# Kernel optimization log

Hardware: AMD Instinct MI355X
Metric: run time of the kernel (lower is better)

## Reference

```python
import jax, jax.numpy as jnp
import numpy as np
import math

SEQ = 45000
FEAT = 30
DEPTH, HEADS, DK, MLP, C = 4, 4, 32, 512, 32
MAXSEQ = 512


def pos_embed_table():
    # Enformer-style basis functions over distances [-SEQ+1, SEQ-1]
    d = jnp.arange(-SEQ + 1, SEQ, dtype=jnp.float32)
    a = jnp.abs(d)[:, None]
    nb = FEAT // 6  # basis per class (exponential / central-mask / gamma)
    # exponential decay
    hl = 2.0 ** jnp.linspace(3.0, math.log(SEQ) / math.log(2.0), nb)
    e1 = jnp.exp(-math.log(2.0) / hl[None, :] * a)
    # central mask
    cw = 2.0 ** jnp.arange(1, nb + 1, dtype=jnp.float32) - 1.0
    e2 = (cw[None, :] > a).astype(jnp.float32)
    # gamma pdf
    stddev = SEQ / (2 * nb)
    start_mean = SEQ / nb
    mean = jnp.linspace(start_mean, float(SEQ), nb)
    conc = (mean / stddev) ** 2
    rate = mean / stddev ** 2
    logp = jax.scipy.special.xlogy(conc - 1.0, a) - rate * a
    logz = jax.scipy.special.gammaln(conc) - conc * jnp.log(rate)
    p = jnp.exp(logp - logz) + 1e-8
    e3 = p / jnp.max(p)
    e = jnp.concatenate([e1, e2, e3], axis=-1)
    return jnp.concatenate([e, jnp.sign(d)[:, None] * e], axis=-1)  # [2*SEQ-1, FEAT]


def layernorm(x, g, b, eps=1e-5):
    mu = jnp.mean(x, axis=-1, keepdims=True)
    var = jnp.var(x, axis=-1, keepdims=True)
    return (x - mu) * jax.lax.rsqrt(var + eps) * g + b


def setup_inputs() -> dict:
    key = jax.random.key(0)
    ks = jax.random.split(key, 16)
    B, L = 2, SEQ
    HD = HEADS * DK
    s = 0.02
    return {
        "x_skip": jax.random.normal(ks[0], (B, C, L), jnp.float32),
        "attention": jax.random.uniform(ks[1], (B, 3, L), jnp.float32),
        "ln1_g": jnp.ones((DEPTH, C), jnp.float32),
        "ln1_b": jnp.zeros((DEPTH, C), jnp.float32),
        "Wq": jax.random.normal(ks[2], (DEPTH, C, HD), jnp.float32) * s,
        "Wk": jax.random.normal(ks[3], (DEPTH, C, HD), jnp.float32) * s,
        "Wv": jax.random.normal(ks[4], (DEPTH, C, HD), jnp.float32) * s,
        "Wrel": jax.random.normal(ks[5], (DEPTH, FEAT, HD), jnp.float32) * s,
        "rcb": jax.random.normal(ks[6], (DEPTH, HEADS, DK), jnp.float32),
        "rpb": jax.random.normal(ks[7], (DEPTH, HEADS, DK), jnp.float32),
        "Wo": jax.random.normal(ks[8], (DEPTH, HD, C), jnp.float32) * s,
        "bo": jnp.zeros((DEPTH, C), jnp.float32),
        "ln2_g": jnp.ones((DEPTH, C), jnp.float32),
        "ln2_b": jnp.zeros((DEPTH, C), jnp.float32),
        "W1": jax.random.normal(ks[9], (DEPTH, C, MLP), jnp.float32) * s,
        "b1": jnp.zeros((DEPTH, MLP), jnp.float32),
        "W2": jax.random.normal(ks[10], (DEPTH, MLP, C), jnp.float32) * s,
        "b2": jnp.zeros((DEPTH, C), jnp.float32),
    }


def reference(x_skip, attention, ln1_g, ln1_b, Wq, Wk, Wv, Wrel, rcb, rpb, Wo, bo, ln2_g, ln2_b, W1, b1, W2, b2):
    B, Cc, L = x_skip.shape
    half = MAXSEQ // 2
    x_emb = jnp.swapaxes(x_skip, 1, 2)  # [B, L, C]
    # top splice sites by acceptor / donor score
    acc = jnp.argsort(-attention[:, 1, :], axis=1)[:, :half]
    don = jnp.argsort(-attention[:, 2, :], axis=1)[:, :half]
    idx = jnp.sort(jnp.concatenate([acc, don], axis=1), axis=1)  # [B, n]
    n = idx.shape[1]
    diff = idx[:, :, None] - idx[:, None, :] + SEQ - 1  # [B, n, n]
    positions = pos_embed_table()[diff]  # [B, n, n, FEAT]
    emb = jnp.take_along_axis(x_emb, idx[:, :, None], axis=1)  # [B, n, C]
    scale = DK ** -0.5
    for l in range(DEPTH):
        h = layernorm(emb, ln1_g[l], ln1_b[l])
        q = (h @ Wq[l]).reshape(B, n, HEADS, DK).transpose(0, 2, 1, 3) * scale
        k = (h @ Wk[l]).reshape(B, n, HEADS, DK).transpose(0, 2, 1, 3)
        v = (h @ Wv[l]).reshape(B, n, HEADS, DK).transpose(0, 2, 1, 3)
        content = jnp.einsum('bhid,bhjd->bhij', q + rcb[l][None, :, None, :], k)
        rel_k = (positions @ Wrel[l]).reshape(B, n, n, HEADS, DK)  # b i j h d
        rel = jnp.einsum('bhid,bijhd->bhij', q + rpb[l][None, :, None, :], rel_k)
        attn_w = jax.nn.softmax(content + rel, axis=-1)
        o = jnp.einsum('bhij,bhjd->bhid', attn_w, v)
        o = o.transpose(0, 2, 1, 3).reshape(B, n, HEADS * DK)
        emb = emb + o @ Wo[l] + bo[l]
        h2 = layernorm(emb, ln2_g[l], ln2_b[l])
        emb = emb + jax.nn.gelu(h2 @ W1[l] + b1[l], approximate=False) @ W2[l] + b2[l]
    out = jnp.zeros_like(x_emb).at[jnp.arange(B)[:, None], idx].set(emb)
    return jnp.swapaxes(out, 1, 2)  # [B, C, L]
```

## Files before the change

### kernel.cpp

```cpp
#include <hip/hip_runtime.h>
#include <math.h>

#define SEQL   45000
#define NBAT   2
#define CCH    32
#define NSEL   512
#define NHEAD  4
#define DKD    32
#define HDD    128
#define MLPD   512
#define CDCAP  2048
#define NSLICE 32
#define ETB    176

__device__ __forceinline__ unsigned short f2bf(float x) {
  unsigned u = __float_as_uint(x);
  u = (u + 0x7fffu + ((u >> 16) & 1u)) >> 16;
  return (unsigned short)u;
}
#define BFL(u) __uint_as_float((u) << 16)
#define BFH(u) __uint_as_float((u) & 0xffff0000u)
#define U8F(w, s) ((float)(((w) >> (s)) & 0xffu))

__global__ __launch_bounds__(256) void prep_kernel(const float* __restrict__ att,
                                                   unsigned char* __restrict__ E,
                                                   int* __restrict__ ghist1,
                                                   float* __restrict__ out) {
  __shared__ int lh[256];
  {
    int nthr = gridDim.x * 256;
    int gt = blockIdx.x * 256 + threadIdx.x;
    float4 z4 = make_float4(0.f, 0.f, 0.f, 0.f);
    float4* o4 = (float4*)out;
    for (int i = gt; i < NBAT * CCH * SEQL / 4; i += nthr) o4[i] = z4;
  }
  if (blockIdx.x < ETB) {
    int a = blockIdx.x * 256 + threadIdx.x;
    if (a >= SEQL) return;
    float ad = (float)a;
    float outv[16];
    float log2S = log2f((float)SEQL);
    #pragma unroll
    for (int k = 0; k < 5; ++k) {
      float hl = exp2f(3.0f + (float)k * (log2S - 3.0f) * 0.25f);
      outv[k] = exp2f(-ad / hl);
    }
    const int cw[5] = {1, 3, 7, 15, 31};
    #pragma unroll
    for (int k = 0; k < 5; ++k) outv[5 + k] = (a < cw[k]) ? 1.0f : 0.0f;
    float pmax = 0.0f;
    float pk[5];
    #pragma unroll
    for (int k = 0; k < 5; ++k) {
      float mean = 9000.0f * (float)(k + 1);
      float sd = 4500.0f;
      float cc = (mean / sd) * (mean / sd);
      float rr = mean / (sd * sd);
      float logz = lgammaf(cc) - cc * logf(rr);
      float pp;
      if (a == 0) pp = 1e-8f;
      else pp = expf((cc - 1.0f) * logf(ad) - rr * ad - logz) + 1e-8f;
      pk[k] = pp;
      float mstar = (cc - 1.0f) / rr;
      float m0 = floorf(mstar), m1 = m0 + 1.0f;
      if (m1 > (float)(SEQL - 1)) m1 = (float)(SEQL - 1);
      float p0 = expf((cc - 1.0f) * logf(m0) - rr * m0 - logz) + 1e-8f;
      float p1 = expf((cc - 1.0f) * logf(m1) - rr * m1 - logz) + 1e-8f;
      pmax = fmaxf(pmax, fmaxf(p0, p1));
    }
    #pragma unroll
    for (int k = 0; k < 5; ++k) outv[10 + k] = pk[k] / pmax;
    outv[15] = 0.0f;
    unsigned by[16];
    #pragma unroll
    for (int k = 0; k < 15; ++k)
      by[k] = (unsigned)(fminf(fmaxf(outv[k], 0.f), 1.f) * 255.f + 0.5f);
    by[15] = 0u;
    uint4 o;
    o.x = by[0]  | (by[1]  << 8) | (by[2]  << 16) | (by[3]  << 24);
    o.y = by[4]  | (by[5]  << 8) | (by[6]  << 16) | (by[7]  << 24);
    o.z = by[8]  | (by[9]  << 8) | (by[10] << 16) | (by[11] << 24);
    o.w = by[12] | (by[13] << 8) | (by[14] << 16);
    *(uint4*)(E + (size_t)a * 16) = o;
  } else {
    int bid = blockIdx.x - ETB;
    int ch4 = bid >> 5, blk = bid & 31;
    int b = ch4 >> 1, ch = ch4 & 1;
    const float* row = att + ((size_t)b * 3 + 1 + ch) * SEQL;
    int t = threadIdx.x;
    lh[t] = 0;
    __syncthreads();
    int per = (SEQL + NSLICE - 1) / NSLICE;
    int lo = blk * per;
    int hi = lo + per; if (hi > SEQL) hi = SEQL;
    for (int i = lo + t; i < hi; i += 256)
      atomicAdd(&lh[__float_as_uint(row[i]) >> 24], 1);
    __syncthreads();
    if (lh[t]) atomicAdd(&ghist1[ch4 * 256 + t], lh[t]);
  }
}

__global__ __launch_bounds__(256) void topk_hist2_kernel(
    const float* __restrict__ att, const int* __restrict__ ghist1,
    int* __restrict__ ghist2) {
  __shared__ int scan[256];
  __shared__ int lh[256];
  __shared__ int auxB;
  int bid = blockIdx.x;
  int ch4 = bid >> 5, blk = bid & 31;
  int b = ch4 >> 1, ch = ch4 & 1;
  const float* row = att + ((size_t)b * 3 + 1 + ch) * SEQL;
  int t = threadIdx.x;
  scan[t] = ghist1[ch4 * 256 + t];
  __syncthreads();
  for (int d = 1; d < 256; d <<= 1) {
    int v = scan[t] + ((t + d < 256) ? scan[t + d] : 0);
    __syncthreads();
    scan[t] = v;
    __syncthreads();
  }
  {
    int sufEx = (t == 255) ? 0 : scan[t + 1];
    if (scan[t] >= 256 && sufEx < 256) auxB = t;
  }
  __syncthreads();
  int B = auxB;
  lh[t] = 0;
  __syncthreads();
  int per = (SEQL + NSLICE - 1) / NSLICE;
  int lo = blk * per;
  int hi = lo + per; if (hi > SEQL) hi = SEQL;
  for (int i = lo + t; i < hi; i += 256) {
    unsigned key = __float_as_uint(row[i]);
    if ((int)(key >> 24) == B) atomicAdd(&lh[(key >> 16) & 0xffu], 1);
  }
  __syncthreads();
  if (lh[t]) atomicAdd(&ghist2[ch4 * 256 + t], lh[t]);
}

__global__ __launch_bounds__(256) void topk_collect_kernel(
    const float* __restrict__ att, const int* __restrict__ ghist1,
    const int* __restrict__ ghist2, unsigned long long* __restrict__ cand,
    int* __restrict__ cnt) {
  __shared__ int scan[256];
  __shared__ int aux[2];
  int bid = blockIdx.x;
  int ch4 = bid >> 5, blk = bid & 31;
  int b = ch4 >> 1, ch = ch4 & 1;
  const float* row = att + ((size_t)b * 3 + 1 + ch) * SEQL;
  int t = threadIdx.x;
  scan[t] = ghist1[ch4 * 256 + t];
  __syncthreads();
  for (int d = 1; d < 256; d <<= 1) {
    int v = scan[t] + ((t + d < 256) ? scan[t + d] : 0);
    __syncthreads();
    scan[t] = v;
    __syncthreads();
  }
  {
    int sufEx = (t == 255) ? 0 : scan[t + 1];
    if (scan[t] >= 256 && sufEx < 256) { aux[0] = t; aux[1] = 256 - sufEx; }
  }
  __syncthreads();
  int B = aux[0], want = aux[1];
  scan[t] = ghist2[ch4 * 256 + t];
  __syncthreads();
  for (int d = 1; d < 256; d <<= 1) {
    int v = scan[t] + ((t + d < 256) ? scan[t + d] : 0);
    __syncthreads();
    scan[t] = v;
    __syncthreads();
  }
  {
    int sufEx = (t == 255) ? 0 : scan[t + 1];
    if (scan[t] >= want && sufEx < want) aux[0] = (B << 8) | t;
  }
  __syncthreads();
  unsigned T16 = (unsigned)aux[0];
  int per = (SEQL + NSLICE - 1) / NSLICE;
  int lo = blk * per;
  int hi = lo + per; if (hi > SEQL) hi = SEQL;
  int lane = t & 63;
  for (int base = lo; base < hi; base += 256) {
    int i = base + t;
    bool pass = false; unsigned key = 0;
    if (i < hi) {
      key = __float_as_uint(row[i]);
      pass = (key >> 16) >= T16;
    }
    unsigned long long mask = __ballot(pass);
    if (mask) {
      int np = __popcll(mask);
      int lead = __ffsll((long long)mask) - 1;
      int pbase = 0;
      if (lane == lead) pbase = atomicAdd(&cnt[ch4], np);
      pbase = __shfl(pbase, lead);
      if (pass) {
        int off = __popcll(mask & ((1ull << lane) - 1ull));
        int p = pbase + off;
        if (p < CDCAP)
          cand[(size_t)ch4 * CDCAP + p] =
              ((unsigned long long)key << 32) | (unsigned)(~(unsigned)i);
      }
    }
  }
}

__global__ __launch_bounds__(1024) void topk_sort_kernel(
    const unsigned long long* __restrict__ cand, const int* __restrict__ cnt,
    unsigned* __restrict__ chsel) {
  __shared__ unsigned long long sc[CDCAP];
  int ch4 = blockIdx.x, t = threadIdx.x;
  int n = cnt[ch4]; if (n > CDCAP) n = CDCAP;
  int P = 256;
  while (P < n) P <<= 1;
  for (int i = t; i < P; i += 1024)
    sc[i] = (i < n) ? cand[(size_t)ch4 * CDCAP + i] : 0ull;
  __syncthreads();
  for (int k = 2; k <= P; k <<= 1) {
    for (int j = k >> 1; j > 0; j >>= 1) {
      for (int i = t; i < P; i += 1024) {
        int ixj = i ^ j;
        if (ixj > i) {
          unsigned long long va = sc[i], vb2 = sc[ixj];
          bool up = ((i & k) == 0);
          if ((va < vb2) == up) { sc[i] = vb2; sc[ixj] = va; }
        }
      }
      __syncthreads();
    }
  }
  if (t < 256)
    chsel[(size_t)ch4 * 256 + t] = ~(unsigned)(sc[t] & 0xFFFFFFFFull);
}

__global__ __launch_bounds__(512) void topk_merge_kernel(const unsigned* __restrict__ chsel,
                                                         int* __restrict__ idx) {
  __shared__ int m[512];
  int b = blockIdx.x, tid = threadIdx.x;
  m[tid] = (int)chsel[(size_t)b * 512 + tid];
  __syncthreads();
  for (int k = 2; k <= 512; k <<= 1) {
    for (int j = k >> 1; j > 0; j >>= 1) {
      int ixj = tid ^ j;
      if (ixj > tid) {
        int va = m[tid], vb2 = m[ixj];
        bool up = ((tid & k) == 0);
        if ((va > vb2) == up) { m[tid] = vb2; m[ixj] = va; }
      }
      __syncthreads();
    }
  }
  idx[b * 512 + tid] = m[tid];
}

__global__ __launch_bounds__(128) void gqkv0_kernel(
    const float* __restrict__ x, const int* __restrict__ idx,
    const float* __restrict__ ln_g, const float* __restrict__ ln_b,
    const float* __restrict__ Wq, const float* __restrict__ Wk,
    const float* __restrict__ Wv, const float* __restrict__ Wrel,
    const float* __restrict__ rcb, const float* __restrict__ rpb,
    float* __restrict__ emb, float* __restrict__ qc,
    unsigned short* __restrict__ kbT, unsigned short* __restrict__ vT,
    float* __restrict__ wb) {
  __shared__ float qs[128];
  const int l = 0;
  int hd = threadIdx.x;
  int hh = hd >> 5, d = hd & 31;
  int row = blockIdx.x;
  int b = row >> 9, ii = row & 511;
  int li = idx[b * NSEL + ii];
  float h[32];
  float mu = 0.f;
  #pragma unroll
  for (int c = 0; c < 32; ++c) {
    h[c] = x[((size_t)b * CCH + c) * SEQL + li];
    mu += h[c];
  }
  if (hd < 32) emb[(size_t)row * CCH + hd] = h[hd];
  mu *= (1.0f / 32.0f);
  float var = 0.f;
  #pragma unroll
  for (int c = 0; c < 32; ++c) { float dd0 = h[c] - mu; var += dd0 * dd0; }
  var *= (1.0f / 32.0f);
  float rstd = rsqrtf(var + 1e-5f);
  const float* g = ln_g + l * CCH;
  const float* bb = ln_b + l * CCH;
  #pragma unroll
  for (int c = 0; c < 32; ++c) h[c] = (h[c] - mu) * rstd * g[c] + bb[c];
  const float* wq = Wq + (size_t)l * CCH * HDD + hd;
  const float* wk = Wk + (size_t)l * CCH * HDD + hd;
  const float* wv = Wv + (size_t)l * CCH * HDD + hd;
  float q = 0.f, kk = 0.f, vv = 0.f;
  #pragma unroll
  for (int c = 0; c < 32; ++c) {
    q += h[c] * wq[c * HDD];
    kk += h[c] * wk[c * HDD];
    vv += h[c] * wv[c * HDD];
  }
  q *= 0.17677669529663687f;
  qs[hd] = q;
  qc[(size_t)row * HDD + hd] = q + rcb[(l * NHEAD + hh) * DKD + d];
  size_t tpos = ((size_t)(b * 4 + hh) * 4 + (d >> 3)) * 4096 + (size_t)ii * 8 + (d & 7);
  kbT[tpos] = f2bf(kk);
  vT[tpos]  = f2bf(vv);
  __syncthreads();
  if (hd < 120) {
    int h2 = hd / 30, f = hd % 30;
    const float* wr = Wrel + ((size_t)l * 30 + f) * HDD + h2 * DKD;
    const float* rp = rpb + (l * NHEAD + h2) * DKD;
    const float* qsh = qs + h2 * DKD;
    float acc = 0.f;
    #pragma unroll
    for (int dd = 0; dd < 32; ++dd) acc += (qsh[dd] + rp[dd]) * wr[dd];
    wb[((size_t)row * NHEAD + h2) * 32 + f] = acc;
  }
}

__global__ __launch_bounds__(256, 4) void layer_kernel(
    const float* __restrict__ qc, const unsigned short* __restrict__ kbT,
    const unsigned short* __restrict__ vT, const float* __restrict__ wbuf,
    const unsigned char* __restrict__ E, const int* __restrict__ idx,
    const float* __restrict__ Wo, const float* __restrict__ bo,
    const float* __restrict__ ln2_g, const float* __restrict__ ln2_b,
    const float* __restrict__ W1, const float* __restrict__ b1,
    const float* __restrict__ W2, const float* __restrict__ b2,
    const float* __restrict__ ln1_g, const float* __restrict__ ln1_b,
    const float* __restrict__ Wq, const float* __restrict__ Wk,
    const float* __restrict__ Wv, const float* __restrict__ Wrel,
    const float* __restrict__ rcb, const float* __restrict__ rpb,
    float* __restrict__ emb, float* __restrict__ qcN,
    unsigned short* __restrict__ kbTN, unsigned short* __restrict__ vTN,
    float* __restrict__ wbN, float* __restrict__ out, int layer) {
  __shared__ float2 es2[8 * 512];
  __shared__ float obs[128];
  __shared__ float part[8][32];
  __shared__ float res[32];
  __shared__ float hln[32];
  __shared__ float fin[32];
  __shared__ float a1s[MLPD];
  __shared__ float qs[128];
  int bid = blockIdx.x;
  int b = bid >> 9;
  int i = bid & 511;
  int tid = threadIdx.x;
  int pos = idx[b * NSEL + i];
  #pragma unroll
  for (int rep = 0; rep < 2; ++rep) {
    int j = tid + rep * 256;
    int dj = pos - idx[b * NSEL + j];
    int a = dj < 0 ? -dj : dj;
    uint4 e = *(const uint4*)(E + (size_t)a * 16);
    float sgn = dj > 0 ? 1.f : (dj < 0 ? -1.f : 0.f);
    es2[0 * 512 + j] = make_float2(U8F(e.x, 0),  U8F(e.x, 8));
    es2[1 * 512 + j] = make_float2(U8F(e.x, 16), U8F(e.x, 24));
    es2[2 * 512 + j] = make_float2(U8F(e.y, 0),  U8F(e.y, 8));
    es2[3 * 512 + j] = make_float2(U8F(e.y, 16), U8F(e.y, 24));
    es2[4 * 512 + j] = make_float2(U8F(e.z, 0),  U8F(e.z, 8));
    es2[5 * 512 + j] = make_float2(U8F(e.z, 16), U8F(e.z, 24));
    es2[6 * 512 + j] = make_float2(U8F(e.w, 0),  U8F(e.w, 8));
    es2[7 * 512 + j] = make_float2(U8F(e.w, 16), sgn);
  }
  __syncthreads();
  {
    int h = tid >> 6, ln = tid & 63;
    const float* qrow = qc + (size_t)(b * NSEL + i) * HDD + h * DKD;
    float q[32];
    #pragma unroll
    for (int d4 = 0; d4 < 8; ++d4) {
      float4 qv = *(const float4*)(qrow + d4 * 4);
      q[d4 * 4 + 0] = qv.x; q[d4 * 4 + 1] = qv.y;
      q[d4 * 4 + 2] = qv.z; q[d4 * 4 + 3] = qv.w;
    }
    const float* wrow = wbuf + ((size_t)(b * NSEL + i) * NHEAD + h) * 32;
    float w0[15], w1[15];
    #pragma unroll
    for (int f = 0; f < 15; ++f) {
      w0[f] = wrow[f] * (1.0f / 255.0f);
      w1[f] = wrow[15 + f] * (1.0f / 255.0f);
    }
    const uint4* kb4 = (const uint4*)kbT + (size_t)(b * 4 + h) * 4 * 512;
    const uint4* vb4 = (const uint4*)vT + (size_t)(b * 4 + h) * 4 * 512;
    float lg[8];
    #pragma unroll
    for (int u = 0; u < 8; ++u) {
      int j = u * 64 + ln;
      float cacc = 0.f;
      #pragma unroll
      for (int dp = 0; dp < 4; ++dp) {
        uint4 kv = kb4[dp * 512 + j];
        cacc += q[dp * 8 + 0] * BFL(kv.x) + q[dp * 8 + 1] * BFH(kv.x)
              + q[dp * 8 + 2] * BFL(kv.y) + q[dp * 8 + 3] * BFH(kv.y)
              + q[dp * 8 + 4] * BFL(kv.z) + q[dp * 8 + 5] * BFH(kv.z)
              + q[dp * 8 + 6] * BFL(kv.w) + q[dp * 8 + 7] * BFH(kv.w);
      }
      float r0 = 0.f, r1 = 0.f;
      float2 e7 = es2[7 * 512 + j];
      #pragma unroll
      for (int f2 = 0; f2 < 7; ++f2) {
        float2 ee = es2[f2 * 512 + j];
        r0 += ee.x * w0[2 * f2] + ee.y * w0[2 * f2 + 1];
        r1 += ee.x * w1[2 * f2] + ee.y * w1[2 * f2 + 1];
      }
      r0 += e7.x * w0[14];
      r1 += e7.x * w1[14];
      lg[u] = cacc + r0 + e7.y * r1;
    }
    float m = lg[0];
    #pragma unroll
    for (int u = 1; u < 8; ++u) m = fmaxf(m, lg[u]);
    #pragma unroll
    for (int s = 1; s < 64; s <<= 1) m = fmaxf(m, __shfl_xor(m, s));
    float ssum = 0.f;
    #pragma unroll
    for (int u = 0; u < 8; ++u) { lg[u] = __expf(lg[u] - m); ssum += lg[u]; }
    #pragma unroll
    for (int s = 1; s < 64; s <<= 1) ssum += __shfl_xor(ssum, s);
    float invs = 1.0f / ssum;
    #pragma unroll
    for (int dp = 0; dp < 4; ++dp) {
      float acc[8] = {0.f, 0.f, 0.f, 0.f, 0.f, 0.f, 0.f, 0.f};
      #pragma unroll
      for (int u = 0; u < 8; ++u) {
        uint4 vv = vb4[dp * 512 + u * 64 + ln];
        float p = lg[u];
        acc[0] += p * BFL(vv.x); acc[1] += p * BFH(vv.x);
        acc[2] += p * BFL(vv.y); acc[3] += p * BFH(vv.y);
        acc[4] += p * BFL(vv.z); acc[5] += p * BFH(vv.z);
        acc[6] += p * BFL(vv.w); acc[7] += p * BFH(vv.w);
      }
      #pragma unroll
      for (int s = 1; s < 8; s <<= 1) {
        #pragma unroll
        for (int t = 0; t < 8; ++t) acc[t] += __shfl_xor(acc[t], s);
      }
      int sel = ln & 7;
      float y = acc[0];
      #pragma unroll
      for (int t = 1; t < 8; ++t) y = (sel == t) ? acc[t] : y;
      #pragma unroll
      for (int s = 8; s < 64; s <<= 1) y += __shfl_xor(y, s);
      if (ln < 8) obs[h * DKD + dp * 8 + ln] = y * invs;
    }
  }
  __syncthreads();
  int c = tid & 31, seg = tid >> 5;
  {
    const float* wo = Wo + (size_t)layer * HDD * CCH + c;
    float pacc = 0.f;
    #pragma unroll
    for (int k = 0; k < 16; ++k) {
      int kk = seg * 16 + k;
      pacc += obs[kk] * wo[kk * CCH];
    }
    part[seg][c] = pacc;
  }
  __syncthreads();
  if (tid < 32) {
    float s = bo[layer * CCH + tid] + emb[(size_t)bid * CCH + tid];
    #pragma unroll
    for (int sg = 0; sg < 8; ++sg) s += part[sg][tid];
    res[tid] = s;
  }
  __syncthreads();
  if (tid < 32) {
    float mu = 0.f, s2 = 0.f;
    #pragma unroll
    for (int c2 = 0; c2 < 32; ++c2) { float v = res[c2]; mu += v; s2 += v * v; }
    mu *= (1.0f / 32.0f);
    float var = s2 * (1.0f / 32.0f) - mu * mu;
    float rstd = rsqrtf(var + 1e-5f);
    hln[tid] = (res[tid] - mu) * rstd * ln2_g[layer * CCH + tid] + ln2_b[layer * CCH + tid];
  }
  __syncthreads();
  {
    const float* w1 = W1 + (size_t)layer * CCH * MLPD;
    float accA = b1[layer * MLPD + tid];
    float accB = b1[layer * MLPD + tid + 256];
    for (int c2 = 0; c2 < 32; ++c2) {
      float hv = hln[c2];
      accA += hv * w1[c2 * MLPD + tid];
      accB += hv * w1[c2 * MLPD + tid + 256];
    }
    a1s[tid]       = 0.5f * accA * (1.0f + erff(accA * 0.70710678118654752f));
    a1s[tid + 256] = 0.5f * accB * (1.0f + erff(accB * 0.70710678118654752f));
  }
  __syncthreads();
  {
    const float* w2 = W2 + (size_t)layer * MLPD * CCH;
    float acc2 = 0.f;
    #pragma unroll 4
    for (int mi = 0; mi < 64; ++mi) {
      int m = seg * 64 + mi;
      acc2 += a1s[m] * w2[m * CCH + c];
    }
    __syncthreads();
    part[seg][c] = acc2;
  }
  __syncthreads();
  if (tid < 32) {
    float s = b2[layer * CCH + tid] + res[tid];
    #pragma unroll
    for (int sg = 0; sg < 8; ++sg) s += part[sg][tid];
    fin[tid] = s;
    if (layer < 3) emb[(size_t)bid * CCH + tid] = s;
  }
  __syncthreads();
  if (layer == 3) {
    if (tid < 32) out[((size_t)b * CCH + tid) * SEQL + pos] = fin[tid];
    return;
  }
  const int l1 = layer + 1;
  bool act = tid < 128;
  int hd = tid & 127;
  int hh2 = hd >> 5, dd2 = hd & 31;
  if (act) {
    float hx[32];
    float mu = 0.f;
    #pragma unroll
    for (int c2 = 0; c2 < 32; ++c2) { hx[c2] = fin[c2]; mu += hx[c2]; }
    mu *= (1.0f / 32.0f);
    float var = 0.f;
    #pragma unroll
    for (int c2 = 0; c2 < 32; ++c2) { float dd = hx[c2] - mu; var += dd * dd; }
    var *= (1.0f / 32.0f);
    float rstd = rsqrtf(var + 1e-5f);
    const float* g = ln1_g + l1 * CCH;
    const float* bb = ln1_b + l1 * CCH;
    #pragma unroll
    for (int c2 = 0; c2 < 32; ++c2) hx[c2] = (hx[c2] - mu) * rstd * g[c2] + bb[c2];
    const float* wq = Wq + (size_t)l1 * CCH * HDD + hd;
    const float* wk = Wk + (size_t)l1 * CCH * HDD + hd;
    const float* wv = Wv + (size_t)l1 * CCH * HDD + hd;
    float q = 0.f, kk = 0.f, vv = 0.f;
    #pragma unroll
    for (int c2 = 0; c2 < 32; ++c2) {
      q += hx[c2] * wq[c2 * HDD];
      kk += hx[c2] * wk[c2 * HDD];
      vv += hx[c2] * wv[c2 * HDD];
    }
    q *= 0.17677669529663687f;
    qs[hd] = q;
    qcN[(size_t)bid * HDD + hd] = q + rcb[(l1 * NHEAD + hh2) * DKD + dd2];
    size_t tpos = ((size_t)(b * 4 + hh2) * 4 + (dd2 >> 3)) * 4096 + (size_t)i * 8 + (dd2 & 7);
    kbTN[tpos] = f2bf(kk);
    vTN[tpos]  = f2bf(vv);
  }
  __syncthreads();
  if (act && hd < 120) {
    int h2 = hd / 30, f = hd % 30;
    const float* rp = rpb + (l1 * NHEAD + h2) * DKD;
    const float* wr = Wrel + ((size_t)l1 * 30 + f) * HDD + h2 * DKD;
    const float* qsh = qs + h2 * DKD;
    float acc = 0.f;
    #pragma unroll
    for (int dd = 0; dd < 32; ++dd) acc += (qsh[dd] + rp[dd]) * wr[dd];
    wbN[((size_t)bid * NHEAD + h2) * 32 + f] = acc;
  }
}

extern "C" void kernel_launch(void* const* d_in, const int* in_sizes, int n_in,
                              void* d_out, int out_size, void* d_ws, size_t ws_size,
                              hipStream_t stream) {
  (void)in_sizes; (void)n_in; (void)ws_size; (void)out_size;
  const float* x_skip    = (const float*)d_in[0];
  const float* attention = (const float*)d_in[1];
  const float* ln1_g = (const float*)d_in[2];
  const float* ln1_b = (const float*)d_in[3];
  const float* Wq    = (const float*)d_in[4];
  const float* Wk    = (const float*)d_in[5];
  const float* Wv    = (const float*)d_in[6];
  const float* Wrel  = (const float*)d_in[7];
  const float* rcb   = (const float*)d_in[8];
  const float* rpb   = (const float*)d_in[9];
  const float* Wo    = (const float*)d_in[10];
  const float* bo    = (const float*)d_in[11];
  const float* ln2_g = (const float*)d_in[12];
  const float* ln2_b = (const float*)d_in[13];
  const float* W1    = (const float*)d_in[14];
  const float* b1    = (const float*)d_in[15];
  const float* W2    = (const float*)d_in[16];
  const float* b2    = (const float*)d_in[17];
  float* out = (float*)d_out;
  char* ws = (char*)d_ws;

  unsigned char* E = (unsigned char*)(ws + 0);
  int*      idx   = (int*)(ws + 1441792);
  float*    emb   = (float*)(ws + 1445888);
  float*    qcA   = (float*)(ws + 1576960);
  unsigned short* kbTA = (unsigned short*)(ws + 2101248);
  unsigned short* vTA  = (unsigned short*)(ws + 2363392);
  float*    wbA   = (float*)(ws + 2625536);
  unsigned short* kbTB = (unsigned short*)(ws + 3149824);
  unsigned short* vTB  = (unsigned short*)(ws + 3411968);
  int*      ghist1 = (int*)(ws + 3674112);
  int*      ghist2 = (int*)(ws + 3678208);
  int*      cnt    = (int*)(ws + 3682304);
  unsigned long long* cand = (unsigned long long*)(ws + 4722720);
  unsigned* chsel = (unsigned*)(ws + 4788256);
  float*    qcB   = (float*)(ws + 4792352);
  float*    wbB   = (float*)(ws + 5316640);

  hipMemsetAsync(ws + 3674112, 0, 4096 + 4096 + 32, stream);
  prep_kernel<<<ETB + 128, 256, 0, stream>>>(attention, E, ghist1, out);
  topk_hist2_kernel<<<128, 256, 0, stream>>>(attention, ghist1, ghist2);
  topk_collect_kernel<<<128, 256, 0, stream>>>(attention, ghist1, ghist2, cand, cnt);
  topk_sort_kernel<<<4, 1024, 0, stream>>>(cand, cnt, chsel);
  topk_merge_kernel<<<2, 512, 0, stream>>>(chsel, idx);
  gqkv0_kernel<<<1024, 128, 0, stream>>>(x_skip, idx, ln1_g, ln1_b, Wq, Wk, Wv,
                                         Wrel, rcb, rpb, emb, qcA, kbTA, vTA, wbA);
  for (int l = 0; l < 4; ++l) {
    const float* qcI = (l & 1) ? qcB : qcA;
    const unsigned short* kbI = (l & 1) ? kbTB : kbTA;
    const unsigned short* vI  = (l & 1) ? vTB : vTA;
    const float* wbI = (l & 1) ? wbB : wbA;
    float* qcO = (l & 1) ? qcA : qcB;
    unsigned short* kbO = (l & 1) ? kbTA : kbTB;
    unsigned short* vO  = (l & 1) ? vTA : vTB;
    float* wbO = (l & 1) ? wbA : wbB;
    layer_kernel<<<1024, 256, 0, stream>>>(qcI, kbI, vI, wbI, E, idx,
                                           Wo, bo, ln2_g, ln2_b, W1, b1, W2, b2,
                                           ln1_g, ln1_b, Wq, Wk, Wv, Wrel, rcb,
                                           rpb, emb, qcO, kbO, vO, wbO, out, l);
  }
}
```

Baseline: 281.9 us.

## Split attention into key-half blocks with flash-style merge in separate kernel

Each layer's attention now runs as a separate kernel over 2048 blocks, each covering half of the keys. It writes a partial PV in bf16 plus the per-head max and sum, and a second kernel merges the two halves with log-sum-exp rescaling before the output projection, MLP and next-layer QKV. The aim is more parallelism and occupancy for the attention phase, since the es2 LDS footprint is halved and launch bounds rise to 6 blocks per CU. The cost is an extra launch per layer, a global round trip for the partials, and the loss of precision from storing unnormalized PV partials in bf16.

Result: slower. 493.0 us (+74.9%).

```diff
diff --git a/kernel.cpp b/kernel.cpp
--- a/kernel.cpp
+++ b/kernel.cpp
@@ -317,10 +317,120 @@
   }
 }
 
-__global__ __launch_bounds__(256, 4) void layer_kernel(
+__global__ __launch_bounds__(256, 6) void attn_half_kernel(
     const float* __restrict__ qc, const unsigned short* __restrict__ kbT,
     const unsigned short* __restrict__ vT, const float* __restrict__ wbuf,
     const unsigned char* __restrict__ E, const int* __restrict__ idx,
+    unsigned short* __restrict__ pvb, float2* __restrict__ msb) {
+  __shared__ float2 es2[8 * 256];
+  int bid = blockIdx.x;
+  int half = bid & 1;
+  int row = bid >> 1;
+  int b = row >> 9;
+  int i = row & 511;
+  int tid = threadIdx.x;
+  int pos = idx[b * NSEL + i];
+  {
+    int j = half * 256 + tid;
+    int dj = pos - idx[b * NSEL + j];
+    int a = dj < 0 ? -dj : dj;
+    uint4 e = *(const uint4*)(E + (size_t)a * 16);
+    float sgn = dj > 0 ? 1.f : (dj < 0 ? -1.f : 0.f);
+    es2[0 * 256 + tid] = make_float2(U8F(e.x, 0),  U8F(e.x, 8));
+    es2[1 * 256 + tid] = make_float2(U8F(e.x, 16), U8F(e.x, 24));
+    es2[2 * 256 + tid] = make_float2(U8F(e.y, 0),  U8F(e.y, 8));
+    es2[3 * 256 + tid] = make_float2(U8F(e.y, 16), U8F(e.y, 24));
+    es2[4 * 256 + tid] = make_float2(U8F(e.z, 0),  U8F(e.z, 8));
+    es2[5 * 256 + tid] = make_float2(U8F(e.z, 16), U8F(e.z, 24));
+    es2[6 * 256 + tid] = make_float2(U8F(e.w, 0),  U8F(e.w, 8));
+    es2[7 * 256 + tid] = make_float2(U8F(e.w, 16), sgn);
+  }
+  __syncthreads();
+  int h = tid >> 6, ln = tid & 63;
+  const float* qrow = qc + (size_t)row * HDD + h * DKD;
+  float q[32];
+  #pragma unroll
+  for (int d4 = 0; d4 < 8; ++d4) {
+    float4 qv = *(const float4*)(qrow + d4 * 4);
+    q[d4 * 4 + 0] = qv.x; q[d4 * 4 + 1] = qv.y;
+    q[d4 * 4 + 2] = qv.z; q[d4 * 4 + 3] = qv.w;
+  }
+  const float* wrow = wbuf + ((size_t)row * NHEAD + h) * 32;
+  float w0[15], w1[15];
+  #pragma unroll
+  for (int f = 0; f < 15; ++f) {
+    w0[f] = wrow[f] * (1.0f / 255.0f);
+    w1[f] = wrow[15 + f] * (1.0f / 255.0f);
+  }
+  const uint4* kb4 = (const uint4*)kbT + (size_t)(b * 4 + h) * 4 * 512;
+  const uint4* vb4 = (const uint4*)vT + (size_t)(b * 4 + h) * 4 * 512;
+  float lg[4];
+  #pragma unroll
+  for (int u = 0; u < 4; ++u) {
+    int jl = u * 64 + ln;
+    int j = half * 256 + jl;
+    float cacc = 0.f;
+    #pragma unroll
+    for (int dp = 0; dp < 4; ++dp) {
+      uint4 kv = kb4[dp * 512 + j];
+      cacc += q[dp * 8 + 0] * BFL(kv.x) + q[dp * 8 + 1] * BFH(kv.x)
+            + q[dp * 8 + 2] * BFL(kv.y) + q[dp * 8 + 3] * BFH(kv.y)
+            + q[dp * 8 + 4] * BFL(kv.z) + q[dp * 8 + 5] * BFH(kv.z)
+            + q[dp * 8 + 6] * BFL(kv.w) + q[dp * 8 + 7] * BFH(kv.w);
+    }
+    float r0 = 0.f, r1 = 0.f;
+    float2 e7 = es2[7 * 256 + jl];
+    #pragma unroll
+    for (int f2 = 0; f2 < 7; ++f2) {
+      float2 ee = es2[f2 * 256 + jl];
+      r0 += ee.x * w0[2 * f2] + ee.y * w0[2 * f2 + 1];
+      r1 += ee.x * w1[2 * f2] + ee.y * w1[2 * f2 + 1];
+    }
+    r0 += e7.x * w0[14];
+    r1 += e7.x * w1[14];
+    lg[u] = cacc + r0 + e7.y * r1;
+  }
+  float m = lg[0];
+  #pragma unroll
+  for (int u = 1; u < 4; ++u) m = fmaxf(m, lg[u]);
+  #pragma unroll
+  for (int s = 1; s < 64; s <<= 1) m = fmaxf(m, __shfl_xor(m, s));
+  float ssum = 0.f;
+  #pragma unroll
+  for (int u = 0; u < 4; ++u) { lg[u] = __expf(lg[u] - m); ssum += lg[u]; }
+  #pragma unroll
+  for (int s = 1; s < 64; s <<= 1) ssum += __shfl_xor(ssum, s);
+  if (ln == 0) msb[(size_t)bid * NHEAD + h] = make_float2(m, ssum);
+  #pragma unroll
+  for (int dp = 0; dp < 4; ++dp) {
+    float acc[8] = {0.f, 0.f, 0.f, 0.f, 0.f, 0.f, 0.f, 0.f};
+    #pragma unroll
+    for (int u = 0; u < 4; ++u) {
+      uint4 vv = vb4[dp * 512 + half * 256 + u * 64 + ln];
+      float p = lg[u];
+      acc[0] += p * BFL(vv.x); acc[1] += p * BFH(vv.x);
+      acc[2] += p * BFL(vv.y); acc[3] += p * BFH(vv.y);
+      acc[4] += p * BFL(vv.z); acc[5] += p * BFH(vv.z);
+      acc[6] += p * BFL(vv.w); acc[7] += p * BFH(vv.w);
+    }
+    #pragma unroll
+    for (int s = 1; s < 8; s <<= 1) {
+      #pragma unroll
+      for (int t = 0; t < 8; ++t) acc[t] += __shfl_xor(acc[t], s);
+    }
+    int sel = ln & 7;
+    float y = acc[0];
+    #pragma unroll
+    for (int t = 1; t < 8; ++t) y = (sel == t) ? acc[t] : y;
+    #pragma unroll
+    for (int s = 8; s < 64; s <<= 1) y += __shfl_xor(y, s);
+    if (ln < 8) pvb[(size_t)bid * HDD + h * DKD + dp * 8 + ln] = f2bf(y);
+  }
+}
+
+__global__ __launch_bounds__(256, 4) void layer2_kernel(
+    const unsigned short* __restrict__ pvb, const float2* __restrict__ msb,
+    const int* __restrict__ idx,
     const float* __restrict__ Wo, const float* __restrict__ bo,
     const float* __restrict__ ln2_g, const float* __restrict__ ln2_b,
     const float* __restrict__ W1, const float* __restrict__ b1,
@@ -332,7 +442,6 @@
     float* __restrict__ emb, float* __restrict__ qcN,
     unsigned short* __restrict__ kbTN, unsigned short* __restrict__ vTN,
     float* __restrict__ wbN, float* __restrict__ out, int layer) {
-  __shared__ float2 es2[8 * 512];
   __shared__ float obs[128];
   __shared__ float part[8][32];
   __shared__ float res[32];
@@ -340,108 +449,20 @@
   __shared__ float fin[32];
   __shared__ float a1s[MLPD];
   __shared__ float qs[128];
-  int bid = blockIdx.x;
-  int b = bid >> 9;
-  int i = bid & 511;
+  int row = blockIdx.x;
+  int b = row >> 9, i = row & 511;
   int tid = threadIdx.x;
   int pos = idx[b * NSEL + i];
-  #pragma unroll
-  for (int rep = 0; rep < 2; ++rep) {
-    int j = tid + rep * 256;
-    int dj = pos - idx[b * NSEL + j];
-    int a = dj < 0 ? -dj : dj;
-    uint4 e = *(const uint4*)(E + (size_t)a * 16);
-    float sgn = dj > 0 ? 1.f : (dj < 0 ? -1.f : 0.f);
-    es2[0 * 512 + j] = make_float2(U8F(e.x, 0),  U8F(e.x, 8));
-    es2[1 * 512 + j] = make_float2(U8F(e.x, 16), U8F(e.x, 24));
-    es2[2 * 512 + j] = make_float2(U8F(e.y, 0),  U8F(e.y, 8));
-    es2[3 * 512 + j] = make_float2(U8F(e.y, 16), U8F(e.y, 24));
-    es2[4 * 512 + j] = make_float2(U8F(e.z, 0),  U8F(e.z, 8));
-    es2[5 * 512 + j] = make_float2(U8F(e.z, 16), U8F(e.z, 24));
-    es2[6 * 512 + j] = make_float2(U8F(e.w, 0),  U8F(e.w, 8));
-    es2[7 * 512 + j] = make_float2(U8F(e.w, 16), sgn);
-  }
-  __syncthreads();
-  {
-    int h = tid >> 6, ln = tid & 63;
-    const float* qrow = qc + (size_t)(b * NSEL + i) * HDD + h * DKD;
-    float q[32];
-    #pragma unroll
-    for (int d4 = 0; d4 < 8; ++d4) {
-      float4 qv = *(const float4*)(qrow + d4 * 4);
-      q[d4 * 4 + 0] = qv.x; q[d4 * 4 + 1] = qv.y;
-      q[d4 * 4 + 2] = qv.z; q[d4 * 4 + 3] = qv.w;
-    }
-    const float* wrow = wbuf + ((size_t)(b * NSEL + i) * NHEAD + h) * 32;
-    float w0[15], w1[15];
-    #pragma unroll
-    for (int f = 0; f < 15; ++f) {
-      w0[f] = wrow[f] * (1.0f / 255.0f);
-      w1[f] = wrow[15 + f] * (1.0f / 255.0f);
-    }
-    const uint4* kb4 = (const uint4*)kbT + (size_t)(b * 4 + h) * 4 * 512;
-    const uint4* vb4 = (const uint4*)vT + (size_t)(b * 4 + h) * 4 * 512;
-    float lg[8];
-    #pragma unroll
-    for (int u = 0; u < 8; ++u) {
-      int j = u * 64 + ln;
-      float cacc = 0.f;
-      #pragma unroll
-      for (int dp = 0; dp < 4; ++dp) {
-        uint4 kv = kb4[dp * 512 + j];
-        cacc += q[dp * 8 + 0] * BFL(kv.x) + q[dp * 8 + 1] * BFH(kv.x)
-              + q[dp * 8 + 2] * BFL(kv.y) + q[dp * 8 + 3] * BFH(kv.y)
-              + q[dp * 8 + 4] * BFL(kv.z) + q[dp * 8 + 5] * BFH(kv.z)
-              + q[dp * 8 + 6] * BFL(kv.w) + q[dp * 8 + 7] * BFH(kv.w);
-      }
-      float r0 = 0.f, r1 = 0.f;
-      float2 e7 = es2[7 * 512 + j];
-      #pragma unroll
-      for (int f2 = 0; f2 < 7; ++f2) {
-        float2 ee = es2[f2 * 512 + j];
-        r0 += ee.x * w0[2 * f2] + ee.y * w0[2 * f2 + 1];
-        r1 += ee.x * w1[2 * f2] + ee.y * w1[2 * f2 + 1];
-      }
-      r0 += e7.x * w0[14];
-      r1 += e7.x * w1[14];
-      lg[u] = cacc + r0 + e7.y * r1;
-    }
-    float m = lg[0];
-    #pragma unroll
-    for (int u = 1; u < 8; ++u) m = fmaxf(m, lg[u]);
-    #pragma unroll
-    for (int s = 1; s < 64; s <<= 1) m = fmaxf(m, __shfl_xor(m, s));
-    float ssum = 0.f;
-    #pragma unroll
-    for (int u = 0; u < 8; ++u) { lg[u] = __expf(lg[u] - m); ssum += lg[u]; }
-    #pragma unroll
-    for (int s = 1; s < 64; s <<= 1) ssum += __shfl_xor(ssum, s);
-    float invs = 1.0f / ssum;
-    #pragma unroll
-    for (int dp = 0; dp < 4; ++dp) {
-      float acc[8] = {0.f, 0.f, 0.f, 0.f, 0.f, 0.f, 0.f, 0.f};
-      #pragma unroll
-      for (int u = 0; u < 8; ++u) {
-        uint4 vv = vb4[dp * 512 + u * 64 + ln];
-        float p = lg[u];
-        acc[0] += p * BFL(vv.x); acc[1] += p * BFH(vv.x);
-        acc[2] += p * BFL(vv.y); acc[3] += p * BFH(vv.y);
-        acc[4] += p * BFL(vv.z); acc[5] += p * BFH(vv.z);
-        acc[6] += p * BFL(vv.w); acc[7] += p * BFH(vv.w);
-      }
-      #pragma unroll
-      for (int s = 1; s < 8; s <<= 1) {
-        #pragma unroll
-        for (int t = 0; t < 8; ++t) acc[t] += __shfl_xor(acc[t], s);
-      }
-      int sel = ln & 7;
-      float y = acc[0];
-      #pragma unroll
-      for (int t = 1; t < 8; ++t) y = (sel == t) ? acc[t] : y;
-      #pragma unroll
-      for (int s = 8; s < 64; s <<= 1) y += __shfl_xor(y, s);
-      if (ln < 8) obs[h * DKD + dp * 8 + ln] = y * invs;
-    }
+  if (tid < 128) {
+    int h = tid >> 5;
+    float2 A  = msb[(size_t)(row * 2 + 0) * NHEAD + h];
+    float2 Bm = msb[(size_t)(row * 2 + 1) * NHEAD + h];
+    float M = fmaxf(A.x, Bm.x);
+    float f0 = __expf(A.x - M), f1 = __expf(Bm.x - M);
+    float inv = 1.0f / (A.y * f0 + Bm.y * f1);
+    float v0 = BFL((unsigned)pvb[(size_t)(row * 2 + 0) * HDD + tid]);
+    float v1 = BFL((unsigned)pvb[(size_t)(row * 2 + 1) * HDD + tid]);
+    obs[tid] = (v0 * f0 + v1 * f1) * inv;
   }
   __syncthreads();
   int c = tid & 31, seg = tid >> 5;
@@ -457,7 +478,7 @@
   }
   __syncthreads();
   if (tid < 32) {
-    float s = bo[layer * CCH + tid] + emb[(size_t)bid * CCH + tid];
+    float s = bo[layer * CCH + tid] + emb[(size_t)row * CCH + tid];
     #pragma unroll
     for (int sg = 0; sg < 8; ++sg) s += part[sg][tid];
     res[tid] = s;
@@ -503,7 +524,7 @@
     #pragma unroll
     for (int sg = 0; sg < 8; ++sg) s += part[sg][tid];
     fin[tid] = s;
-    if (layer < 3) emb[(size_t)bid * CCH + tid] = s;
+    if (layer < 3) emb[(size_t)row * CCH + tid] = s;
   }
   __syncthreads();
   if (layer == 3) {
@@ -541,7 +562,7 @@
     }
     q *= 0.17677669529663687f;
     qs[hd] = q;
-    qcN[(size_t)bid * HDD + hd] = q + rcb[(l1 * NHEAD + hh2) * DKD + dd2];
+    qcN[(size_t)row * HDD + hd] = q + rcb[(l1 * NHEAD + hh2) * DKD + dd2];
     size_t tpos = ((size_t)(b * 4 + hh2) * 4 + (dd2 >> 3)) * 4096 + (size_t)i * 8 + (dd2 & 7);
     kbTN[tpos] = f2bf(kk);
     vTN[tpos]  = f2bf(vv);
@@ -555,7 +576,7 @@
     float acc = 0.f;
     #pragma unroll
     for (int dd = 0; dd < 32; ++dd) acc += (qsh[dd] + rp[dd]) * wr[dd];
-    wbN[((size_t)bid * NHEAD + h2) * 32 + f] = acc;
+    wbN[((size_t)row * NHEAD + h2) * 32 + f] = acc;
   }
 }
 
@@ -596,6 +617,8 @@
   int*      ghist1 = (int*)(ws + 3674112);
   int*      ghist2 = (int*)(ws + 3678208);
   int*      cnt    = (int*)(ws + 3682304);
+  unsigned short* pvb = (unsigned short*)(ws + 3682336);
+  float2*   msb   = (float2*)(ws + 4206624);
   unsigned long long* cand = (unsigned long long*)(ws + 4722720);
   unsigned* chsel = (unsigned*)(ws + 4788256);
   float*    qcB   = (float*)(ws + 4792352);
@@ -618,9 +641,11 @@
     unsigned short* kbO = (l & 1) ? kbTA : kbTB;
     unsigned short* vO  = (l & 1) ? vTA : vTB;
     float* wbO = (l & 1) ? wbA : wbB;
-    layer_kernel<<<1024, 256, 0, stream>>>(qcI, kbI, vI, wbI, E, idx,
-                                           Wo, bo, ln2_g, ln2_b, W1, b1, W2, b2,
-                                           ln1_g, ln1_b, Wq, Wk, Wv, Wrel, rcb,
-                                           rpb, emb, qcO, kbO, vO, wbO, out, l);
-  }
-}
+    attn_half_kernel<<<2048, 256, 0, stream>>>(qcI, kbI, vI, wbI, E, idx,
+                                               pvb, msb);
+    layer2_kernel<<<1024, 256, 0, stream>>>(pvb, msb, idx,
+                                            Wo, bo, ln2_g, ln2_b, W1, b1, W2, b2,
+                                            ln1_g, ln1_b, Wq, Wk, Wv, Wrel, rcb,
+                                            rpb, emb, qcO, kbO, vO, wbO, out, l);
+  }
+}
```
